# Performance work log

Measured on AMD Instinct MI355X. Metric: run time of the kernel, lower is better.

The kernel has to match this reference:

```python
import jax, jax.numpy as jnp
import numpy as np

B, S, D = 4, 2048, 1024
KEY_DIM, VALUE_DIM = 1024, 1024
BETA = 1.0 / np.sqrt(D)  # beta defaults to 1/sqrt(input dim), per build()


def setup_inputs() -> dict:
    key = jax.random.key(0)
    ks = jax.random.split(key, 9)
    inv = 1.0 / np.sqrt(D)
    return {
        "query": jax.random.normal(ks[0], (B, S, D), dtype=jnp.float32),
        "key": jax.random.normal(ks[1], (B, S, D), dtype=jnp.float32),
        "value": jax.random.normal(ks[2], (B, S, D), dtype=jnp.float32),
        "Wq": jax.random.normal(ks[3], (D, KEY_DIM), dtype=jnp.float32) * inv,
        "bq": jnp.zeros((KEY_DIM,), dtype=jnp.float32),
        "Wk": jax.random.normal(ks[4], (D, KEY_DIM), dtype=jnp.float32) * inv,
        "bk": jnp.zeros((KEY_DIM,), dtype=jnp.float32),
        "Wv": jax.random.normal(ks[5], (D, VALUE_DIM), dtype=jnp.float32) * inv,
        "bv": jnp.zeros((VALUE_DIM,), dtype=jnp.float32),
    }


def reference(query, key, value, Wq, bq, Wk, bk, Wv, bv):
    # Dense projections
    q = query @ Wq + bq          # [B, S, key_dim]
    k = key @ Wk + bk            # [B, S, key_dim]
    v = value @ Wv + bv          # [B, S, value_dim]
    # Scaled dot-product attention (beta applied AFTER matmul, as in source)
    scores = jnp.einsum("bik,bjk->bij", q, k)  # [B, S, S]
    A = jax.nn.softmax(BETA * scores, axis=-1)
    return jnp.einsum("bij,bjk->bik", A, v)    # [B, S, value_dim]
```

## Files before the change

### kernel.cpp

```cpp
#include <hip/hip_runtime.h>


typedef __bf16 bf16x8 __attribute__((ext_vector_type(8)));
typedef float f32x4 __attribute__((ext_vector_type(4)));

#define MIB ((size_t)1 << 20)

__device__ __forceinline__ unsigned short f2b(float f) {
  unsigned int u = __float_as_uint(f);
  return (unsigned short)((u + 0x7FFFu + ((u >> 16) & 1u)) >> 16);
}

__device__ __forceinline__ void async16(const void* g, void* l) {
  __builtin_amdgcn_global_load_lds(
      (const __attribute__((address_space(1))) unsigned int*)g,
      (__attribute__((address_space(3))) unsigned int*)l, 16, 0, 0);
}

template <int TN>
__device__ __forceinline__ void gemm_loop(
    const unsigned short* __restrict__ A, const unsigned short* __restrict__ Bt,
    unsigned short* lds_a, unsigned short* lds_b, int K, int m0, int n0,
    f32x4 (&acc)[4][TN / 32]) {
  constexpr int NI = TN / 32;
  const int tid = threadIdx.x;
  const int lane = tid & 63;
  const int wave = tid >> 6;
  const int wm = (wave >> 1) * 64;
  const int wn = (wave & 1) * (TN / 2);
  const int fr = lane & 15;
  const int q = lane >> 4;

  for (int kb = 0; kb < K; kb += 64) {
#pragma unroll
    for (int i = 0; i < 4; ++i) {
      const int e = i * 256 + tid;
      const int r = e >> 3;
      const int cg = (e & 7) ^ (r & 7);
      async16(A + (size_t)(m0 + r) * K + kb + cg * 8, &lds_a[e * 8]);
    }
#pragma unroll
    for (int i = 0; i < TN / 32; ++i) {
      const int e = i * 256 + tid;
      const int r = e >> 3;
      const int cg = (e & 7) ^ (r & 7);
      async16(Bt + (size_t)(n0 + r) * K + kb + cg * 8, &lds_b[e * 8]);
    }
    __syncthreads();

#pragma unroll
    for (int ks = 0; ks < 64; ks += 32) {
      const int kc = (ks >> 3) + q;
      bf16x8 av[4], bv[NI];
#pragma unroll
      for (int mi = 0; mi < 4; ++mi) {
        const int R = wm + mi * 16 + fr;
        av[mi] = *(const bf16x8*)&lds_a[R * 64 + ((kc ^ (R & 7)) << 3)];
      }
#pragma unroll
      for (int ni = 0; ni < NI; ++ni) {
        const int R = wn + ni * 16 + fr;
        bv[ni] = *(const bf16x8*)&lds_b[R * 64 + ((kc ^ (R & 7)) << 3)];
      }
#pragma unroll
      for (int mi = 0; mi < 4; ++mi)
#pragma unroll
        for (int ni = 0; ni < NI; ++ni)
          acc[mi][ni] = __builtin_amdgcn_mfma_f32_16x16x32_bf16(
              av[mi], bv[ni], acc[mi][ni], 0, 0, 0);
    }
    __syncthreads();
  }
}

struct ProjArgs {
  const unsigned short* A[3];
  const unsigned short* Bt[3];
  unsigned short* C[3];
  const float* bias[3];
};

__global__ __launch_bounds__(256) void proj_gemm(ProjArgs p) {
  __shared__ __align__(16) unsigned short lds_a[128 * 64];
  __shared__ __align__(16) unsigned short lds_b[128 * 64];

  const int z = blockIdx.z;
  const int m0 = blockIdx.y * 128;
  const int n0 = blockIdx.x * 128;

  f32x4 acc[4][4] = {};
  gemm_loop<128>(p.A[z], p.Bt[z], lds_a, lds_b, 1024, m0, n0, acc);

  const int lane = threadIdx.x & 63;
  const int wave = threadIdx.x >> 6;
  const int wm = (wave >> 1) * 64;
  const int wn = (wave & 1) * 64;
  const int fr = lane & 15;
  const float* bias = p.bias[z];

  if (z != 2) {
    unsigned short* C = p.C[z];
#pragma unroll
    for (int mi = 0; mi < 4; ++mi) {
#pragma unroll
      for (int ni = 0; ni < 4; ++ni) {
        const int col = n0 + wn + ni * 16 + fr;
        const float bb = bias[col];
        const int rowb = m0 + wm + mi * 16 + (lane >> 4) * 4;
#pragma unroll
        for (int r = 0; r < 4; ++r)
          C[(size_t)(rowb + r) * 1024 + col] = f2b(acc[mi][ni][r] + bb);
      }
    }
  } else {
    unsigned short* C = p.C[2] + (size_t)(m0 >> 11) * (2048 * 1024);
#pragma unroll
    for (int mi = 0; mi < 4; ++mi) {
#pragma unroll
      for (int ni = 0; ni < 4; ++ni) {
        const int col = n0 + wn + ni * 16 + fr;
        const float bb = bias[col];
        const int rowb = (m0 + wm + mi * 16 + (lane >> 4) * 4) & 2047;
        ushort4 o = make_ushort4(f2b(acc[mi][ni][0] + bb), f2b(acc[mi][ni][1] + bb),
                                 f2b(acc[mi][ni][2] + bb), f2b(acc[mi][ni][3] + bb));
        *(ushort4*)&C[(size_t)col * 2048 + rowb] = o;
      }
    }
  }
}

template <int TN>
__global__ __launch_bounds__(256) void gemm_f32(
    const unsigned short* __restrict__ A, const unsigned short* __restrict__ Bt,
    float* __restrict__ C, int K, int ldc, long long sA, long long sB,
    long long sC) {
  __shared__ __align__(16) unsigned short lds_a[128 * 64];
  __shared__ __align__(16) unsigned short lds_b[TN * 64];
  const int bz = blockIdx.z;
  A += (long long)bz * sA;
  Bt += (long long)bz * sB;
  C += (long long)bz * sC;
  const int m0 = blockIdx.y * 128;
  const int n0 = blockIdx.x * TN;

  f32x4 acc[4][TN / 32] = {};
  gemm_loop<TN>(A, Bt, lds_a, lds_b, K, m0, n0, acc);

  const int lane = threadIdx.x & 63;
  const int wave = threadIdx.x >> 6;
  const int wm = (wave >> 1) * 64;
  const int wn = (wave & 1) * (TN / 2);
  const int fr = lane & 15;
#pragma unroll
  for (int mi = 0; mi < 4; ++mi) {
#pragma unroll
    for (int ni = 0; ni < TN / 32; ++ni) {
      const int col = n0 + wn + ni * 16 + fr;
      const int rowb = m0 + wm + mi * 16 + (lane >> 4) * 4;
#pragma unroll
      for (int r = 0; r < 4; ++r)
        C[(size_t)(rowb + r) * ldc + col] = acc[mi][ni][r];
    }
  }
}

__global__ __launch_bounds__(256) void cast3(
    const float4* __restrict__ a, const float4* __restrict__ b,
    const float4* __restrict__ c, ushort4* __restrict__ oa,
    ushort4* __restrict__ ob, ushort4* __restrict__ oc, int n4) {
  const int i = blockIdx.x * 256 + threadIdx.x;
  if (i >= n4) return;
  const float4* src = (blockIdx.y == 0) ? a : (blockIdx.y == 1) ? b : c;
  ushort4* dst = (blockIdx.y == 0) ? oa : (blockIdx.y == 1) ? ob : oc;
  float4 v = src[i];
  dst[i] = make_ushort4(f2b(v.x), f2b(v.y), f2b(v.z), f2b(v.w));
}

__global__ __launch_bounds__(256) void transpose3(
    const float* __restrict__ w0, const float* __restrict__ w1,
    const float* __restrict__ w2, unsigned short* __restrict__ t0,
    unsigned short* __restrict__ t1, unsigned short* __restrict__ t2) {
  __shared__ float t[32][33];
  const int K = 1024, N = 1024;
  const float* W = (blockIdx.z == 0) ? w0 : (blockIdx.z == 1) ? w1 : w2;
  unsigned short* WT = (blockIdx.z == 0) ? t0 : (blockIdx.z == 1) ? t1 : t2;
  const int n0 = blockIdx.x * 32, k0 = blockIdx.y * 32;
  const int tx = threadIdx.x, ty = threadIdx.y;
#pragma unroll
  for (int i = 0; i < 32; i += 8)
    t[ty + i][tx] = W[(size_t)(k0 + ty + i) * N + (n0 + tx)];
  __syncthreads();
#pragma unroll
  for (int i = 0; i < 32; i += 8)
    WT[(size_t)(n0 + ty + i) * K + (k0 + tx)] = f2b(t[tx][ty + i]);
}

__global__ __launch_bounds__(256) void softmax_rows(const float* __restrict__ S,
                                                    unsigned short* __restrict__ P) {
  const int cols = 2048;
  const size_t row = blockIdx.x;
  const float4* srow = (const float4*)(S + row * cols);
  const int tid = threadIdx.x;
  const int lane = tid & 63;
  const int wave = tid >> 6;

  float4 a = srow[tid];
  float4 b = srow[tid + 256];

  float mx = fmaxf(fmaxf(fmaxf(a.x, a.y), fmaxf(a.z, a.w)),
                   fmaxf(fmaxf(b.x, b.y), fmaxf(b.z, b.w)));
#pragma unroll
  for (int o = 1; o < 64; o <<= 1) mx = fmaxf(mx, __shfl_xor(mx, o));

  __shared__ float red[8];
  if (lane == 0) red[wave] = mx;
  __syncthreads();
  mx = fmaxf(fmaxf(red[0], red[1]), fmaxf(red[2], red[3]));

  const float c = 0.03125f * 1.4426950408889634f;
  float4 pa, pb;
  pa.x = exp2f((a.x - mx) * c); pa.y = exp2f((a.y - mx) * c);
  pa.z = exp2f((a.z - mx) * c); pa.w = exp2f((a.w - mx) * c);
  pb.x = exp2f((b.x - mx) * c); pb.y = exp2f((b.y - mx) * c);
  pb.z = exp2f((b.z - mx) * c); pb.w = exp2f((b.w - mx) * c);

  float sum = pa.x + pa.y + pa.z + pa.w + pb.x + pb.y + pb.z + pb.w;
#pragma unroll
  for (int o = 1; o < 64; o <<= 1) sum += __shfl_xor(sum, o);
  if (lane == 0) red[4 + wave] = sum;
  __syncthreads();
  sum = red[4] + red[5] + red[6] + red[7];

  const float inv = 1.0f / sum;
  ushort4* prow = (ushort4*)(P + row * cols);
  prow[tid] = make_ushort4(f2b(pa.x * inv), f2b(pa.y * inv), f2b(pa.z * inv),
                           f2b(pa.w * inv));
  prow[tid + 256] = make_ushort4(f2b(pb.x * inv), f2b(pb.y * inv),
                                 f2b(pb.z * inv), f2b(pb.w * inv));
}

extern "C" void kernel_launch(void* const* d_in, const int* in_sizes, int n_in,
                              void* d_out, int out_size, void* d_ws, size_t ws_size,
                              hipStream_t stream) {
  const float* query = (const float*)d_in[0];
  const float* key_ = (const float*)d_in[1];
  const float* value = (const float*)d_in[2];
  const float* Wq = (const float*)d_in[3];
  const float* bq = (const float*)d_in[4];
  const float* Wk = (const float*)d_in[5];
  const float* bk = (const float*)d_in[6];
  const float* Wv = (const float*)d_in[7];
  const float* bv = (const float*)d_in[8];
  float* out = (float*)d_out;

  char* ws = (char*)d_ws;
  unsigned short* WqT = (unsigned short*)ws;
  unsigned short* WkT = WqT + (size_t)1024 * 1024;
  unsigned short* WvT = WkT + (size_t)1024 * 1024;
  unsigned short* Xq = (unsigned short*)(ws + 6 * MIB);
  unsigned short* Xk = Xq + (size_t)8192 * 1024;
  unsigned short* Xv = Xk + (size_t)8192 * 1024;
  unsigned short* qb = (unsigned short*)(ws + 54 * MIB);
  unsigned short* kb = (unsigned short*)(ws + 70 * MIB);
  unsigned short* vT = (unsigned short*)(ws + 86 * MIB);
  float* sc = (float*)(ws + 102 * MIB);
  unsigned short* P = (unsigned short*)(ws + 6 * MIB);

  const int n4 = (4 * 2048 * 1024) / 4;
  cast3<<<dim3(n4 / 256, 3), 256, 0, stream>>>(
      (const float4*)query, (const float4*)key_, (const float4*)value,
      (ushort4*)Xq, (ushort4*)Xk, (ushort4*)Xv, n4);

  transpose3<<<dim3(32, 32, 3), dim3(32, 8), 0, stream>>>(Wq, Wk, Wv, WqT, WkT,
                                                          WvT);

  ProjArgs pa;
  pa.A[0] = Xq;  pa.A[1] = Xk;  pa.A[2] = Xv;
  pa.Bt[0] = WqT; pa.Bt[1] = WkT; pa.Bt[2] = WvT;
  pa.C[0] = qb;  pa.C[1] = kb;  pa.C[2] = vT;
  pa.bias[0] = bq; pa.bias[1] = bk; pa.bias[2] = bv;
  proj_gemm<<<dim3(8, 64, 3), 256, 0, stream>>>(pa);

  gemm_f32<128><<<dim3(16, 16, 4), 256, 0, stream>>>(
      qb, kb, sc, 1024, 2048, 2048LL * 1024, 2048LL * 1024, 2048LL * 2048);

  softmax_rows<<<8192, 256, 0, stream>>>(sc, P);

  gemm_f32<128><<<dim3(8, 16, 4), 256, 0, stream>>>(
      P, vT, out, 2048, 1024, 2048LL * 2048, 1024LL * 2048, 2048LL * 1024);
}
```

Measured before the change: 344.0 us.

## Double-buffer GEMM LDS tiles and swap MFMA operands for vectorized row stores

The shared GEMM loop now stages tiles into two LDS buffers, prefetching tile t+1 while MFMAs run on tile t. LDS reads use precomputed offsets with inline ds_read_b128 followed by a single waitcnt. MFMA operands are swapped for row-major outputs, so each lane holds four consecutive columns and can write them with one vector store (float4 or ushort4). The projection kernel is split into a Q/K launch and a V launch, which doubles LDS per block (64 KB) and may reduce occupancy.

```diff
diff --git a/kernel.cpp b/kernel.cpp
--- a/kernel.cpp
+++ b/kernel.cpp
@@ -17,12 +17,42 @@
       (__attribute__((address_space(3))) unsigned int*)l, 16, 0, 0);
 }
 
+__device__ __forceinline__ unsigned ldsoff(const unsigned short* p) {
+  return (unsigned)(size_t)(const __attribute__((address_space(3))) unsigned short*)p;
+}
+
+__device__ __forceinline__ bf16x8 ds_read16(unsigned off) {
+  bf16x8 r;
+  asm volatile("ds_read_b128 %0, %1" : "=v"(r) : "v"(off));
+  return r;
+}
+
 template <int TN>
+__device__ __forceinline__ void stage_tile(
+    const unsigned short* __restrict__ A, const unsigned short* __restrict__ Bt,
+    unsigned short* dst, int K, int kb, int tid) {
+#pragma unroll
+  for (int i = 0; i < 4; ++i) {
+    const int e = i * 256 + tid;
+    const int r = e >> 3;
+    const int cg = (e & 7) ^ (r & 7);
+    async16(A + (size_t)r * K + kb + cg * 8, dst + e * 8);
+  }
+#pragma unroll
+  for (int i = 0; i < TN / 32; ++i) {
+    const int e = i * 256 + tid;
+    const int r = e >> 3;
+    const int cg = (e & 7) ^ (r & 7);
+    async16(Bt + (size_t)r * K + kb + cg * 8, dst + 128 * 64 + e * 8);
+  }
+}
+
+template <int TN, bool SWAP>
 __device__ __forceinline__ void gemm_loop(
     const unsigned short* __restrict__ A, const unsigned short* __restrict__ Bt,
-    unsigned short* lds_a, unsigned short* lds_b, int K, int m0, int n0,
-    f32x4 (&acc)[4][TN / 32]) {
+    unsigned short* lds, int K, int m0, int n0, f32x4 (&acc)[4][TN / 32]) {
   constexpr int NI = TN / 32;
+  constexpr unsigned BUFB = (128 + TN) * 64 * 2;
   const int tid = threadIdx.x;
   const int lane = tid & 63;
   const int wave = tid >> 6;
@@ -30,45 +60,66 @@
   const int wn = (wave & 1) * (TN / 2);
   const int fr = lane & 15;
   const int q = lane >> 4;
-
-  for (int kb = 0; kb < K; kb += 64) {
-#pragma unroll
-    for (int i = 0; i < 4; ++i) {
-      const int e = i * 256 + tid;
-      const int r = e >> 3;
-      const int cg = (e & 7) ^ (r & 7);
-      async16(A + (size_t)(m0 + r) * K + kb + cg * 8, &lds_a[e * 8]);
-    }
-#pragma unroll
-    for (int i = 0; i < TN / 32; ++i) {
-      const int e = i * 256 + tid;
-      const int r = e >> 3;
-      const int cg = (e & 7) ^ (r & 7);
-      async16(Bt + (size_t)(n0 + r) * K + kb + cg * 8, &lds_b[e * 8]);
-    }
-    __syncthreads();
-
-#pragma unroll
-    for (int ks = 0; ks < 64; ks += 32) {
-      const int kc = (ks >> 3) + q;
-      bf16x8 av[4], bv[NI];
-#pragma unroll
-      for (int mi = 0; mi < 4; ++mi) {
-        const int R = wm + mi * 16 + fr;
-        av[mi] = *(const bf16x8*)&lds_a[R * 64 + ((kc ^ (R & 7)) << 3)];
-      }
-#pragma unroll
-      for (int ni = 0; ni < NI; ++ni) {
-        const int R = wn + ni * 16 + fr;
-        bv[ni] = *(const bf16x8*)&lds_b[R * 64 + ((kc ^ (R & 7)) << 3)];
-      }
+  const int NT = K >> 6;
+
+  const unsigned short* Ab = A + (size_t)m0 * K;
+  const unsigned short* Bb = Bt + (size_t)n0 * K;
+  const unsigned LB = ldsoff(lds);
+
+  unsigned oa[4][2], ob[NI][2];
+#pragma unroll
+  for (int mi = 0; mi < 4; ++mi) {
+    const int R = wm + mi * 16 + fr;
+#pragma unroll
+    for (int ks = 0; ks < 2; ++ks) {
+      const int kc = ks * 4 + q;
+      oa[mi][ks] = (unsigned)((R * 64 + ((kc ^ (R & 7)) << 3)) * 2);
+    }
+  }
+#pragma unroll
+  for (int ni = 0; ni < NI; ++ni) {
+    const int R = wn + ni * 16 + fr;
+#pragma unroll
+    for (int ks = 0; ks < 2; ++ks) {
+      const int kc = ks * 4 + q;
+      ob[ni][ks] =
+          (unsigned)(128 * 64 * 2 + (R * 64 + ((kc ^ (R & 7)) << 3)) * 2);
+    }
+  }
+
+  stage_tile<TN>(Ab, Bb, lds, K, 0, tid);
+  __syncthreads();
+
+  for (int t = 0; t < NT; ++t) {
+    const unsigned boff = LB + (unsigned)(t & 1) * BUFB;
+    if (t + 1 < NT)
+      stage_tile<TN>(Ab, Bb, lds + ((t + 1) & 1) * (BUFB / 2), K,
+                     (t + 1) << 6, tid);
+
+    bf16x8 av[2][4], bv[2][NI];
+#pragma unroll
+    for (int ks = 0; ks < 2; ++ks)
+#pragma unroll
+      for (int mi = 0; mi < 4; ++mi) av[ks][mi] = ds_read16(boff + oa[mi][ks]);
+#pragma unroll
+    for (int ks = 0; ks < 2; ++ks)
+#pragma unroll
+      for (int ni = 0; ni < NI; ++ni) bv[ks][ni] = ds_read16(boff + ob[ni][ks]);
+
+    asm volatile("s_waitcnt lgkmcnt(0)");
+    __builtin_amdgcn_sched_barrier(0);
+
+#pragma unroll
+    for (int ks = 0; ks < 2; ++ks)
 #pragma unroll
       for (int mi = 0; mi < 4; ++mi)
 #pragma unroll
         for (int ni = 0; ni < NI; ++ni)
-          acc[mi][ni] = __builtin_amdgcn_mfma_f32_16x16x32_bf16(
-              av[mi], bv[ni], acc[mi][ni], 0, 0, 0);
-    }
+          acc[mi][ni] = SWAP ? __builtin_amdgcn_mfma_f32_16x16x32_bf16(
+                                   bv[ks][ni], av[ks][mi], acc[mi][ni], 0, 0, 0)
+                             : __builtin_amdgcn_mfma_f32_16x16x32_bf16(
+                                   av[ks][mi], bv[ks][ni], acc[mi][ni], 0, 0, 0);
+
     __syncthreads();
   }
 }
@@ -80,86 +131,99 @@
   const float* bias[3];
 };
 
-__global__ __launch_bounds__(256) void proj_gemm(ProjArgs p) {
-  __shared__ __align__(16) unsigned short lds_a[128 * 64];
-  __shared__ __align__(16) unsigned short lds_b[128 * 64];
-
+__global__ __launch_bounds__(256) void proj_qk(ProjArgs p) {
+  __shared__ __align__(16) unsigned short lds[2 * 256 * 64];
   const int z = blockIdx.z;
   const int m0 = blockIdx.y * 128;
   const int n0 = blockIdx.x * 128;
 
   f32x4 acc[4][4] = {};
-  gemm_loop<128>(p.A[z], p.Bt[z], lds_a, lds_b, 1024, m0, n0, acc);
+  gemm_loop<128, true>(p.A[z], p.Bt[z], lds, 1024, m0, n0, acc);
 
   const int lane = threadIdx.x & 63;
   const int wave = threadIdx.x >> 6;
   const int wm = (wave >> 1) * 64;
   const int wn = (wave & 1) * 64;
   const int fr = lane & 15;
+  const int q4 = (lane >> 4) * 4;
   const float* bias = p.bias[z];
-
-  if (z != 2) {
-    unsigned short* C = p.C[z];
-#pragma unroll
-    for (int mi = 0; mi < 4; ++mi) {
-#pragma unroll
-      for (int ni = 0; ni < 4; ++ni) {
-        const int col = n0 + wn + ni * 16 + fr;
-        const float bb = bias[col];
-        const int rowb = m0 + wm + mi * 16 + (lane >> 4) * 4;
-#pragma unroll
-        for (int r = 0; r < 4; ++r)
-          C[(size_t)(rowb + r) * 1024 + col] = f2b(acc[mi][ni][r] + bb);
-      }
-    }
-  } else {
-    unsigned short* C = p.C[2] + (size_t)(m0 >> 11) * (2048 * 1024);
-#pragma unroll
-    for (int mi = 0; mi < 4; ++mi) {
-#pragma unroll
-      for (int ni = 0; ni < 4; ++ni) {
-        const int col = n0 + wn + ni * 16 + fr;
-        const float bb = bias[col];
-        const int rowb = (m0 + wm + mi * 16 + (lane >> 4) * 4) & 2047;
-        ushort4 o = make_ushort4(f2b(acc[mi][ni][0] + bb), f2b(acc[mi][ni][1] + bb),
-                                 f2b(acc[mi][ni][2] + bb), f2b(acc[mi][ni][3] + bb));
-        *(ushort4*)&C[(size_t)col * 2048 + rowb] = o;
-      }
-    }
-  }
-}
-
-template <int TN>
+  unsigned short* C = p.C[z];
+
+#pragma unroll
+  for (int mi = 0; mi < 4; ++mi) {
+    const int m = m0 + wm + mi * 16 + fr;
+#pragma unroll
+    for (int ni = 0; ni < 4; ++ni) {
+      const int nb = n0 + wn + ni * 16 + q4;
+      const float4 bb = *(const float4*)&bias[nb];
+      ushort4 o = make_ushort4(
+          f2b(acc[mi][ni][0] + bb.x), f2b(acc[mi][ni][1] + bb.y),
+          f2b(acc[mi][ni][2] + bb.z), f2b(acc[mi][ni][3] + bb.w));
+      *(ushort4*)&C[(size_t)m * 1024 + nb] = o;
+    }
+  }
+}
+
+__global__ __launch_bounds__(256) void proj_v(ProjArgs p) {
+  __shared__ __align__(16) unsigned short lds[2 * 256 * 64];
+  const int m0 = blockIdx.y * 128;
+  const int n0 = blockIdx.x * 128;
+
+  f32x4 acc[4][4] = {};
+  gemm_loop<128, false>(p.A[2], p.Bt[2], lds, 1024, m0, n0, acc);
+
+  const int lane = threadIdx.x & 63;
+  const int wave = threadIdx.x >> 6;
+  const int wm = (wave >> 1) * 64;
+  const int wn = (wave & 1) * 64;
+  const int fr = lane & 15;
+  const int q4 = (lane >> 4) * 4;
+  const float* bias = p.bias[2];
+
+  unsigned short* C = p.C[2] + (size_t)(m0 >> 11) * (2048 * 1024);
+#pragma unroll
+  for (int mi = 0; mi < 4; ++mi) {
+#pragma unroll
+    for (int ni = 0; ni < 4; ++ni) {
+      const int col = n0 + wn + ni * 16 + fr;
+      const float bb = bias[col];
+      const int rowb = (m0 + wm + mi * 16 + q4) & 2047;
+      ushort4 o =
+          make_ushort4(f2b(acc[mi][ni][0] + bb), f2b(acc[mi][ni][1] + bb),
+                       f2b(acc[mi][ni][2] + bb), f2b(acc[mi][ni][3] + bb));
+      *(ushort4*)&C[(size_t)col * 2048 + rowb] = o;
+    }
+  }
+}
+
 __global__ __launch_bounds__(256) void gemm_f32(
     const unsigned short* __restrict__ A, const unsigned short* __restrict__ Bt,
     float* __restrict__ C, int K, int ldc, long long sA, long long sB,
     long long sC) {
-  __shared__ __align__(16) unsigned short lds_a[128 * 64];
-  __shared__ __align__(16) unsigned short lds_b[TN * 64];
+  __shared__ __align__(16) unsigned short lds[2 * 256 * 64];
   const int bz = blockIdx.z;
   A += (long long)bz * sA;
   Bt += (long long)bz * sB;
   C += (long long)bz * sC;
   const int m0 = blockIdx.y * 128;
-  const int n0 = blockIdx.x * TN;
-
-  f32x4 acc[4][TN / 32] = {};
-  gemm_loop<TN>(A, Bt, lds_a, lds_b, K, m0, n0, acc);
+  const int n0 = blockIdx.x * 128;
+
+  f32x4 acc[4][4] = {};
+  gemm_loop<128, true>(A, Bt, lds, K, m0, n0, acc);
 
   const int lane = threadIdx.x & 63;
   const int wave = threadIdx.x >> 6;
   const int wm = (wave >> 1) * 64;
-  const int wn = (wave & 1) * (TN / 2);
+  const int wn = (wave & 1) * 64;
   const int fr = lane & 15;
+  const int q4 = (lane >> 4) * 4;
 #pragma unroll
   for (int mi = 0; mi < 4; ++mi) {
-#pragma unroll
-    for (int ni = 0; ni < TN / 32; ++ni) {
-      const int col = n0 + wn + ni * 16 + fr;
-      const int rowb = m0 + wm + mi * 16 + (lane >> 4) * 4;
-#pragma unroll
-      for (int r = 0; r < 4; ++r)
-        C[(size_t)(rowb + r) * ldc + col] = acc[mi][ni][r];
+    const int m = m0 + wm + mi * 16 + fr;
+#pragma unroll
+    for (int ni = 0; ni < 4; ++ni) {
+      const int nb = n0 + wn + ni * 16 + q4;
+      *(f32x4*)&C[(size_t)m * ldc + nb] = acc[mi][ni];
     }
   }
 }
@@ -279,13 +343,15 @@
   pa.Bt[0] = WqT; pa.Bt[1] = WkT; pa.Bt[2] = WvT;
   pa.C[0] = qb;  pa.C[1] = kb;  pa.C[2] = vT;
   pa.bias[0] = bq; pa.bias[1] = bk; pa.bias[2] = bv;
-  proj_gemm<<<dim3(8, 64, 3), 256, 0, stream>>>(pa);
-
-  gemm_f32<128><<<dim3(16, 16, 4), 256, 0, stream>>>(
+
+  proj_qk<<<dim3(8, 64, 2), 256, 0, stream>>>(pa);
+  proj_v<<<dim3(8, 64, 1), 256, 0, stream>>>(pa);
+
+  gemm_f32<<<dim3(16, 16, 4), 256, 0, stream>>>(
       qb, kb, sc, 1024, 2048, 2048LL * 1024, 2048LL * 1024, 2048LL * 2048);
 
   softmax_rows<<<8192, 256, 0, stream>>>(sc, P);
 
-  gemm_f32<128><<<dim3(8, 16, 4), 256, 0, stream>>>(
+  gemm_f32<<<dim3(8, 16, 4), 256, 0, stream>>>(
       P, vT, out, 2048, 1024, 2048LL * 2048, 1024LL * 2048, 2048LL * 1024);
 }
```

Result: no change. 337.4 us (-1.9%).
